# Kernel tuning notes

Measured on AMD Instinct MI355X. Metric: run time of the kernel, lower is better.

## Reference

```python
import jax, jax.numpy as jnp
import numpy as np

N_NODES = 50000
N_GRAPHS = 512

def _glorot(key, shape):
    fan_in, fan_out = shape[1], shape[0]
    lim = np.sqrt(6.0 / (fan_in + fan_out))
    return jax.random.uniform(key, shape, jnp.float32, -lim, lim)

def setup_inputs() -> dict:
    key = jax.random.key(0)
    ks = jax.random.split(key, 12)
    x = jax.random.normal(ks[0], (N_NODES, 128), jnp.float32)
    edge_index = jax.random.randint(ks[1], (2, 800000), 0, N_NODES, jnp.int64)
    batch = jnp.sort(jax.random.randint(ks[2], (N_NODES,), 0, N_GRAPHS, jnp.int64))
    return {
        "x": x,
        "edge_index": edge_index,
        "batch": batch,
        "W1": _glorot(ks[3], (256, 128)), "b1": jnp.zeros((256,), jnp.float32),
        "W2": _glorot(ks[4], (256, 256)), "b2": jnp.zeros((256,), jnp.float32),
        "W3": _glorot(ks[5], (256, 256)), "b3": jnp.zeros((256,), jnp.float32),
        "Wf1": _glorot(ks[6], (128, 256)), "bf1": jnp.zeros((128,), jnp.float32),
        "Wf2": _glorot(ks[7], (10, 128)), "bf2": jnp.zeros((10,), jnp.float32),
    }

def _gin_conv(h, edge_index, W, b):
    # GINConv (eps=0): lin(x_i + sum_{j in N(i)} x_j)
    src, dst = edge_index[0], edge_index[1]
    aggr = jax.ops.segment_sum(h[src], dst, num_segments=N_NODES)
    return (h + aggr) @ W.T + b

def reference(x, edge_index, batch, W1, b1, W2, b2, W3, b3, Wf1, bf1, Wf2, bf2):
    h = jax.nn.relu(_gin_conv(x, edge_index, W1, b1))
    h = jax.nn.relu(_gin_conv(h, edge_index, W2, b2))
    h = jax.nn.relu(_gin_conv(h, edge_index, W3, b3))
    # global mean pool over graphs
    sums = jax.ops.segment_sum(h, batch, num_segments=N_GRAPHS)
    counts = jax.ops.segment_sum(jnp.ones((N_NODES,), h.dtype), batch, num_segments=N_GRAPHS)
    hg = sums / jnp.maximum(counts, 1.0)[:, None]
    h = jax.nn.relu(hg @ Wf1.T + bf1)
    return h @ Wf2.T + bf2
```

## Files before the change

### kernel.cpp

```cpp
#include <hip/hip_runtime.h>

#define N_NODES 50000
#define N_GRAPHS 512
#define N_EDGES 800000

typedef __attribute__((ext_vector_type(8))) short short8;
typedef __attribute__((ext_vector_type(8))) unsigned short ushort8;
typedef __attribute__((ext_vector_type(4))) float floatx4;
typedef __attribute__((ext_vector_type(2))) float floatx2;

__device__ __forceinline__ float bf2f(unsigned short u) {
    union { unsigned int i; float f; } c;
    c.i = ((unsigned int)u) << 16;
    return c.f;
}
__device__ __forceinline__ unsigned short f2bf(float f) {
    union { float f; unsigned int i; } c;
    c.f = f;
    unsigned int u = c.i;
    return (unsigned short)((u + 0x7fffu + ((u >> 16) & 1u)) >> 16);
}

__device__ __forceinline__ unsigned char ftofp8(float f) {
    union { float f; unsigned int u; } c; c.f = f;
    unsigned int s = (c.u >> 24) & 0x80u;
    float a = fabsf(f);
    if (a < 0x1p-6f) return (unsigned char)s;
    if (a > 448.f)   return (unsigned char)(s | 0x7E);
    unsigned int u = c.u & 0x7FFFFFFFu;
    unsigned int r = u + 0x7FFFFu + ((u >> 20) & 1u);
    return (unsigned char)(s | (((r >> 23) - 120u) << 3) | ((r >> 20) & 7u));
}

__device__ __forceinline__ void f8acc(float* acc, uint2 v) {
    floatx2 a = __builtin_amdgcn_cvt_pk_f32_fp8(v.x, false);
    floatx2 b = __builtin_amdgcn_cvt_pk_f32_fp8(v.x, true);
    floatx2 c = __builtin_amdgcn_cvt_pk_f32_fp8(v.y, false);
    floatx2 d = __builtin_amdgcn_cvt_pk_f32_fp8(v.y, true);
    acc[0] += a[0]; acc[1] += a[1]; acc[2] += b[0]; acc[3] += b[1];
    acc[4] += c[0]; acc[5] += c[1]; acc[6] += d[0]; acc[7] += d[1];
}

__device__ __forceinline__ void g2lds16(const unsigned short* g, void* lds) {
    __builtin_amdgcn_global_load_lds(
        (const __attribute__((address_space(1))) void*)g,
        (__attribute__((address_space(3))) void*)lds, 16, 0, 0);
}

__global__ void conv_deg(const float* __restrict__ x, const float* __restrict__ W1,
                         const float* __restrict__ W2, const float* __restrict__ W3,
                         const int* __restrict__ dst,
                         unsigned char* __restrict__ xf8, unsigned short* __restrict__ o1,
                         unsigned short* __restrict__ o2, unsigned short* __restrict__ o3,
                         int* __restrict__ deg, float4* __restrict__ sums4) {
    int i = blockIdx.x * blockDim.x + threadIdx.x;
    if (i >= 2440960) {
        int j = i - 2440960;
        if (j < 32768) sums4[j] = make_float4(0.f, 0.f, 0.f, 0.f);
        return;
    }
    if (i >= 1640960) {
        int e = i - 1640960;
        atomicAdd(&deg[dst[e]], 1);
        return;
    }
    if (i < 1600000) {
        float4 v = ((const float4*)x)[i];
        uchar4 o;
        o.x = ftofp8(v.x); o.y = ftofp8(v.y); o.z = ftofp8(v.z); o.w = ftofp8(v.w);
        ((uchar4*)xf8)[i] = o;
        return;
    }
    int j = i - 1600000;
    const float* src; unsigned short* out; int base;
    if (j < 8192)       { src = W1; out = o1; base = j; }
    else if (j < 24576) { src = W2; out = o2; base = j - 8192; }
    else                { src = W3; out = o3; base = j - 24576; }
    float4 v = ((const float4*)src)[base];
    ushort4 o;
    o.x = f2bf(v.x); o.y = f2bf(v.y); o.z = f2bf(v.z); o.w = f2bf(v.w);
    ((ushort4*)out)[base] = o;
}

__global__ __launch_bounds__(1024) void scan1(const int* __restrict__ deg,
                                              int* __restrict__ rowptr,
                                              int* __restrict__ blocksum) {
    __shared__ int s[1024];
    int t = threadIdx.x;
    int i = blockIdx.x * 1024 + t;
    int v = (i < N_NODES) ? deg[i] : 0;
    s[t] = v;
    __syncthreads();
    for (int off = 1; off < 1024; off <<= 1) {
        int add = (t >= off) ? s[t - off] : 0;
        __syncthreads();
        s[t] += add;
        __syncthreads();
    }
    if (i < N_NODES) rowptr[i] = s[t] - v;
    if (t == 1023) blocksum[blockIdx.x] = s[t];
}

__global__ __launch_bounds__(1024) void scan3(int* __restrict__ rowptr,
                                              const int* __restrict__ blocksum,
                                              int* __restrict__ cursor) {
    __shared__ int bse[64];
    int t = threadIdx.x;
    if (t < 64) {
        const int NB = (N_NODES + 1023) / 1024;
        int orig = (t < NB) ? blocksum[t] : 0;
        int v = orig;
        for (int off = 1; off < 64; off <<= 1) {
            int u = __shfl_up(v, off, 64);
            if (t >= off) v += u;
        }
        bse[t] = v - orig;
    }
    __syncthreads();
    int i = blockIdx.x * 1024 + t;
    if (i < N_NODES) {
        int v = rowptr[i] + bse[i >> 10];
        rowptr[i] = v;
        cursor[i] = v;
    }
    if (i == 0) rowptr[N_NODES] = N_EDGES;
}

__global__ void scatter_csr(const int* __restrict__ src, const int* __restrict__ dst,
                            int* __restrict__ cursor, int* __restrict__ csr) {
    int e = blockIdx.x * blockDim.x + threadIdx.x;
    if (e < N_EDGES) {
        int pos = atomicAdd(&cursor[dst[e]], 1);
        csr[pos] = src[e];
    }
}

template <int C>
__global__ __launch_bounds__(256) void gather_f8(const unsigned char* __restrict__ h,
                                                 const int* __restrict__ rowptr,
                                                 const int* __restrict__ csr,
                                                 unsigned short* __restrict__ agg) {
    const int TPN = C / 8;
    const int NPB = 256 / TPN;
    int t = threadIdx.x;
    int n = blockIdx.x * NPB + t / TPN;
    if (n >= N_NODES) return;
    int c8 = t % TPN;
    const uint2* hp = (const uint2*)h + c8;
    float acc[8];
#pragma unroll
    for (int j = 0; j < 8; j++) acc[j] = 0.f;
    f8acc(acc, hp[(size_t)n * TPN]);
    int p = rowptr[n], end = rowptr[n + 1];
    for (; p + 8 <= end; p += 8) {
        int j0 = csr[p],     j1 = csr[p + 1], j2 = csr[p + 2], j3 = csr[p + 3];
        int j4 = csr[p + 4], j5 = csr[p + 5], j6 = csr[p + 6], j7 = csr[p + 7];
        uint2 v0 = hp[(size_t)j0 * TPN];
        uint2 v1 = hp[(size_t)j1 * TPN];
        uint2 v2 = hp[(size_t)j2 * TPN];
        uint2 v3 = hp[(size_t)j3 * TPN];
        uint2 v4 = hp[(size_t)j4 * TPN];
        uint2 v5 = hp[(size_t)j5 * TPN];
        uint2 v6 = hp[(size_t)j6 * TPN];
        uint2 v7 = hp[(size_t)j7 * TPN];
        f8acc(acc, v0); f8acc(acc, v1); f8acc(acc, v2); f8acc(acc, v3);
        f8acc(acc, v4); f8acc(acc, v5); f8acc(acc, v6); f8acc(acc, v7);
    }
    for (; p + 4 <= end; p += 4) {
        int j0 = csr[p], j1 = csr[p + 1], j2 = csr[p + 2], j3 = csr[p + 3];
        uint2 v0 = hp[(size_t)j0 * TPN];
        uint2 v1 = hp[(size_t)j1 * TPN];
        uint2 v2 = hp[(size_t)j2 * TPN];
        uint2 v3 = hp[(size_t)j3 * TPN];
        f8acc(acc, v0); f8acc(acc, v1); f8acc(acc, v2); f8acc(acc, v3);
    }
    for (; p < end; ++p) {
        uint2 v = hp[(size_t)csr[p] * TPN];
        f8acc(acc, v);
    }
    ushort8 o;
#pragma unroll
    for (int j = 0; j < 8; j++) o[j] = f2bf(acc[j]);
    ((ushort8*)agg)[(size_t)n * TPN + c8] = o;
}

template <int K, int F8OUT>
__global__ __launch_bounds__(256) void gemm_mfma64(
    const unsigned short* __restrict__ A, const unsigned short* __restrict__ W,
    const float* __restrict__ bias, void* __restrict__ Cout, int M) {
    __shared__ short8 As[256];
    __shared__ short8 Ws[512];

    int tid = threadIdx.x;
    int wave = tid >> 6, lane = tid & 63;
    int wm = wave & 1, wn = wave >> 1;
    int rowbase = blockIdx.x * 64;
    int colbase = blockIdx.y * 128;
    int lkc = lane >> 4, lr = lane & 15;
    int rsw = lr ^ (lkc << 2);
    int rslot = lkc * 16 + rsw;

    int ar = rowbase + wave * 16 + rsw; if (ar >= M) ar = M - 1;
    int wr0 = colbase + (0 * 4 + wave) * 16 + rsw;
    int wr1 = colbase + (1 * 4 + wave) * 16 + rsw;
    char* asb  = (char*)As + (size_t)(wave * 64) * 16;
    char* wsb0 = (char*)Ws + (size_t)(0 * 256 + wave * 64) * 16;
    char* wsb1 = (char*)Ws + (size_t)(1 * 256 + wave * 64) * 16;

    floatx4 acc[2][4];
#pragma unroll
    for (int i = 0; i < 2; i++)
#pragma unroll
        for (int j = 0; j < 4; j++) acc[i][j] = (floatx4)(0.f);

#pragma unroll 2
    for (int k0 = 0; k0 < K; k0 += 32) {
        int ks = k0 + lkc * 8;
        g2lds16(A + (size_t)ar * K + ks, asb);
        g2lds16(W + (size_t)wr0 * K + ks, wsb0);
        g2lds16(W + (size_t)wr1 * K + ks, wsb1);
        __syncthreads();

        short8 af[2], wf[4];
#pragma unroll
        for (int mt = 0; mt < 2; mt++) af[mt] = As[(wm * 2 + mt) * 64 + rslot];
#pragma unroll
        for (int nt = 0; nt < 4; nt++) wf[nt] = Ws[(wn * 4 + nt) * 64 + rslot];
#pragma unroll
        for (int mt = 0; mt < 2; mt++)
#pragma unroll
            for (int nt = 0; nt < 4; nt++)
                acc[mt][nt] = __builtin_amdgcn_mfma_f32_16x16x32_bf16(
                    af[mt], wf[nt], acc[mt][nt], 0, 0, 0);
        __syncthreads();
    }

#pragma unroll
    for (int mt = 0; mt < 2; mt++) {
#pragma unroll
        for (int reg = 0; reg < 4; reg++) {
            int row = rowbase + (wm * 2 + mt) * 16 + lkc * 4 + reg;
            if (row >= M) continue;
#pragma unroll
            for (int nt = 0; nt < 4; nt++) {
                int col = colbase + (wn * 4 + nt) * 16 + lr;
                float v = fmaxf(acc[mt][nt][reg] + bias[col], 0.f);
                if (F8OUT)
                    ((unsigned char*)Cout)[(size_t)row * 256 + col] = ftofp8(v);
                else
                    ((unsigned short*)Cout)[(size_t)row * 256 + col] = f2bf(v);
            }
        }
    }
}

__global__ __launch_bounds__(256) void pool_accum(const unsigned short* __restrict__ h,
                                                  const int* __restrict__ batch,
                                                  float* __restrict__ sums) {
    int t = threadIdx.x;
    int r0 = blockIdx.x * 32;
    int r1 = r0 + 32; if (r1 > N_NODES) r1 = N_NODES;
    if (r0 >= N_NODES) return;
    float acc = 0.f;
    int gcur = batch[r0];
    for (int r = r0; r < r1; ++r) {
        int g = batch[r];
        if (g != gcur) { atomicAdd(&sums[gcur * 256 + t], acc); acc = 0.f; gcur = g; }
        acc += bf2f(h[(size_t)r * 256 + t]);
    }
    atomicAdd(&sums[gcur * 256 + t], acc);
}

__global__ __launch_bounds__(128) void head(const float* __restrict__ sums,
                                            const int* __restrict__ batch,
                                            const float* __restrict__ Wf1,
                                            const float* __restrict__ bf1,
                                            const float* __restrict__ Wf2,
                                            const float* __restrict__ bf2,
                                            float* __restrict__ out) {
    __shared__ float hg[256];
    __shared__ float hid[128];
    int g = blockIdx.x;
    int t = threadIdx.x;
    int lo = 0, hi = N_NODES;
    while (lo < hi) { int m = (lo + hi) >> 1; if (batch[m] < g) lo = m + 1; else hi = m; }
    int start = lo;
    lo = 0; hi = N_NODES;
    while (lo < hi) { int m = (lo + hi) >> 1; if (batch[m] < g + 1) lo = m + 1; else hi = m; }
    int end = lo;
    float inv = 1.0f / fmaxf((float)(end - start), 1.0f);
    hg[t]       = sums[g * 256 + t] * inv;
    hg[t + 128] = sums[g * 256 + t + 128] * inv;
    __syncthreads();
    float a1 = bf1[t];
    for (int c = 0; c < 256; c++) a1 += hg[c] * Wf1[t * 256 + c];
    hid[t] = fmaxf(a1, 0.f);
    __syncthreads();
    if (t < 10) {
        float a = bf2[t];
        for (int j = 0; j < 128; j++) a += hid[j] * Wf2[t * 128 + j];
        out[g * 10 + t] = a;
    }
}

extern "C" void kernel_launch(void* const* d_in, const int* in_sizes, int n_in,
                              void* d_out, int out_size, void* d_ws, size_t ws_size,
                              hipStream_t stream) {
    const float* x   = (const float*)d_in[0];
    const int*  edge = (const int*)d_in[1];
    const int*  batch= (const int*)d_in[2];
    const float* W1  = (const float*)d_in[3];
    const float* b1  = (const float*)d_in[4];
    const float* W2  = (const float*)d_in[5];
    const float* b2  = (const float*)d_in[6];
    const float* W3  = (const float*)d_in[7];
    const float* b3  = (const float*)d_in[8];
    const float* Wf1 = (const float*)d_in[9];
    const float* bf1 = (const float*)d_in[10];
    const float* Wf2 = (const float*)d_in[11];
    const float* bf2 = (const float*)d_in[12];
    const int* src = edge;
    const int* dst = edge + N_EDGES;

    char* wsb = (char*)d_ws;
    size_t off = 0;
    auto alloc = [&](size_t bytes) { void* p = wsb + off; off += (bytes + 255) & ~(size_t)255; return p; };
    unsigned char*  x_f8  = (unsigned char*)alloc((size_t)N_NODES * 128);
    unsigned char*  h1_f8 = (unsigned char*)alloc((size_t)N_NODES * 256);
    unsigned char*  h2_f8 = (unsigned char*)alloc((size_t)N_NODES * 256);
    unsigned short* agg_bf= (unsigned short*)alloc((size_t)N_NODES * 256 * 2);
    unsigned short* hA_bf = (unsigned short*)alloc((size_t)N_NODES * 256 * 2);
    unsigned short* W1bf  = (unsigned short*)alloc(256 * 128 * 2);
    unsigned short* W2bf  = (unsigned short*)alloc(256 * 256 * 2);
    unsigned short* W3bf  = (unsigned short*)alloc(256 * 256 * 2);
    int* rowptr   = (int*)alloc((N_NODES + 4) * 4);
    int* cursor   = (int*)alloc(N_NODES * 4);
    int* deg      = (int*)alloc(N_NODES * 4);
    int* csr      = (int*)alloc(N_EDGES * 4);
    int* blocksum = (int*)alloc(64 * 4);
    float* sums   = (float*)alloc((size_t)N_GRAPHS * 256 * 4);

    const int NB_SCAN = (N_NODES + 1023) / 1024;

    hipMemsetAsync(deg, 0, N_NODES * sizeof(int), stream);
    conv_deg<<<(2473728 + 255) / 256, 256, 0, stream>>>(
        x, W1, W2, W3, dst, x_f8, W1bf, W2bf, W3bf, deg, (float4*)sums);

    scan1<<<NB_SCAN, 1024, 0, stream>>>(deg, rowptr, blocksum);
    scan3<<<NB_SCAN, 1024, 0, stream>>>(rowptr, blocksum, cursor);
    scatter_csr<<<(N_EDGES + 255) / 256, 256, 0, stream>>>(src, dst, cursor, csr);

    dim3 ggrid((N_NODES + 63) / 64, 2);

    gather_f8<128><<<(N_NODES + 15) / 16, 256, 0, stream>>>(x_f8, rowptr, csr, agg_bf);
    gemm_mfma64<128, 1><<<ggrid, 256, 0, stream>>>(agg_bf, W1bf, b1, h1_f8, N_NODES);

    gather_f8<256><<<(N_NODES + 7) / 8, 256, 0, stream>>>(h1_f8, rowptr, csr, agg_bf);
    gemm_mfma64<256, 1><<<ggrid, 256, 0, stream>>>(agg_bf, W2bf, b2, h2_f8, N_NODES);

    gather_f8<256><<<(N_NODES + 7) / 8, 256, 0, stream>>>(h2_f8, rowptr, csr, agg_bf);
    gemm_mfma64<256, 0><<<ggrid, 256, 0, stream>>>(agg_bf, W3bf, b3, hA_bf, N_NODES);

    pool_accum<<<(N_NODES + 31) / 32, 256, 0, stream>>>(hA_bf, batch, sums);
    head<<<N_GRAPHS, 128, 0, stream>>>(sums, batch, Wf1, bf1, Wf2, bf2, (float*)d_out);
}
```

Measured before the change: 380.4 us.

## Build CSR via two-pass bucketed binning and store 16-bit column indices

Replaces the single-pass global-atomic CSR scatter with a two-phase scheme: edges are first binned into 49 destination buckets of 1024 nodes using shared-memory counters and one global atomic per bucket per block. A per-bucket pass then scatters them into the CSR, so the per-node cursor atomics and writes stay within a localized region. CSR column indices shrink to 16-bit, which cuts the index bytes the gather kernels read. The 16-bit packing truncates node IDs at or above 65536, which fits only because N_NODES is 50000, and it adds a staging buffer and an extra launch. The scatter pass uses just 49 blocks, which may underuse the GPU.

```diff
diff --git a/kernel.cpp b/kernel.cpp
--- a/kernel.cpp
+++ b/kernel.cpp
@@ -3,6 +3,7 @@
 #define N_NODES 50000
 #define N_GRAPHS 512
 #define N_EDGES 800000
+#define NBKT 49
 
 typedef __attribute__((ext_vector_type(8))) short short8;
 typedef __attribute__((ext_vector_type(8))) unsigned short ushort8;
@@ -103,7 +104,8 @@
 
 __global__ __launch_bounds__(1024) void scan3(int* __restrict__ rowptr,
                                               const int* __restrict__ blocksum,
-                                              int* __restrict__ cursor) {
+                                              int* __restrict__ cursor,
+                                              int* __restrict__ gcursor) {
     __shared__ int bse[64];
     int t = threadIdx.x;
     if (t < 64) {
@@ -122,23 +124,62 @@
         int v = rowptr[i] + bse[i >> 10];
         rowptr[i] = v;
         cursor[i] = v;
+        if ((i & 1023) == 0) gcursor[i >> 10] = v;
     }
     if (i == 0) rowptr[N_NODES] = N_EDGES;
 }
 
-__global__ void scatter_csr(const int* __restrict__ src, const int* __restrict__ dst,
-                            int* __restrict__ cursor, int* __restrict__ csr) {
-    int e = blockIdx.x * blockDim.x + threadIdx.x;
-    if (e < N_EDGES) {
-        int pos = atomicAdd(&cursor[dst[e]], 1);
-        csr[pos] = src[e];
+__global__ __launch_bounds__(256) void bin_edges(const int* __restrict__ src,
+                                                 const int* __restrict__ dst,
+                                                 int* __restrict__ gcursor,
+                                                 unsigned int* __restrict__ staging) {
+    __shared__ int cnt[NBKT];
+    __shared__ int base[NBKT];
+    int t = threadIdx.x;
+    if (t < NBKT) cnt[t] = 0;
+    __syncthreads();
+    int e0 = blockIdx.x * 2048;
+    int d[8], s[8];
+#pragma unroll
+    for (int r = 0; r < 8; r++) {
+        int e = e0 + r * 256 + t;
+        if (e < N_EDGES) {
+            d[r] = dst[e]; s[r] = src[e];
+            atomicAdd(&cnt[d[r] >> 10], 1);
+        } else d[r] = -1;
+    }
+    __syncthreads();
+    if (t < NBKT) base[t] = atomicAdd(&gcursor[t], cnt[t]);
+    __syncthreads();
+#pragma unroll
+    for (int r = 0; r < 8; r++) {
+        if (d[r] >= 0) {
+            int off = atomicAdd(&base[d[r] >> 10], 1);
+            staging[off] = ((unsigned)d[r] << 16) | (unsigned)s[r];
+        }
+    }
+}
+
+__global__ __launch_bounds__(1024) void scatter_bkt(const unsigned int* __restrict__ staging,
+                                                    const int* __restrict__ rowptr,
+                                                    int* __restrict__ cursor,
+                                                    unsigned short* __restrict__ csr) {
+    int b = blockIdx.x;
+    int lo = rowptr[b << 10];
+    int nhi = (b + 1) << 10; if (nhi > N_NODES) nhi = N_NODES;
+    int hi = rowptr[nhi];
+    for (int p = lo + threadIdx.x; p < hi; p += 1024) {
+        unsigned v = staging[p];
+        int d = v >> 16;
+        int pos = atomicAdd(&cursor[d], 1);
+        csr[pos] = (unsigned short)(v & 0xFFFFu);
     }
 }
 
 template <int C>
 __global__ __launch_bounds__(256) void gather_f8(const unsigned char* __restrict__ h,
                                                  const int* __restrict__ rowptr,
-                                                 const int* __restrict__ csr,
+                                                 const unsigned short* __restrict__ csr,
                                                  unsigned short* __restrict__ agg) {
     const int TPN = C / 8;
     const int NPB = 256 / TPN;
@@ -325,20 +366,22 @@
     char* wsb = (char*)d_ws;
     size_t off = 0;
     auto alloc = [&](size_t bytes) { void* p = wsb + off; off += (bytes + 255) & ~(size_t)255; return p; };
-    unsigned char*  x_f8  = (unsigned char*)alloc((size_t)N_NODES * 128);
-    unsigned char*  h1_f8 = (unsigned char*)alloc((size_t)N_NODES * 256);
-    unsigned char*  h2_f8 = (unsigned char*)alloc((size_t)N_NODES * 256);
-    unsigned short* agg_bf= (unsigned short*)alloc((size_t)N_NODES * 256 * 2);
-    unsigned short* hA_bf = (unsigned short*)alloc((size_t)N_NODES * 256 * 2);
-    unsigned short* W1bf  = (unsigned short*)alloc(256 * 128 * 2);
-    unsigned short* W2bf  = (unsigned short*)alloc(256 * 256 * 2);
-    unsigned short* W3bf  = (unsigned short*)alloc(256 * 256 * 2);
-    int* rowptr   = (int*)alloc((N_NODES + 4) * 4);
-    int* cursor   = (int*)alloc(N_NODES * 4);
-    int* deg      = (int*)alloc(N_NODES * 4);
-    int* csr      = (int*)alloc(N_EDGES * 4);
-    int* blocksum = (int*)alloc(64 * 4);
-    float* sums   = (float*)alloc((size_t)N_GRAPHS * 256 * 4);
+    unsigned char*  x_f8   = (unsigned char*)alloc((size_t)N_NODES * 128);
+    unsigned char*  h1_f8  = (unsigned char*)alloc((size_t)N_NODES * 256);
+    unsigned char*  h2_f8  = (unsigned char*)alloc((size_t)N_NODES * 256);
+    unsigned short* agg_bf = (unsigned short*)alloc((size_t)N_NODES * 256 * 2);
+    unsigned short* hA_bf  = (unsigned short*)alloc((size_t)N_NODES * 256 * 2);
+    unsigned short* W1bf   = (unsigned short*)alloc(256 * 128 * 2);
+    unsigned short* W2bf   = (unsigned short*)alloc(256 * 256 * 2);
+    unsigned short* W3bf   = (unsigned short*)alloc(256 * 256 * 2);
+    int* rowptr    = (int*)alloc((N_NODES + 4) * 4);
+    int* cursor    = (int*)alloc(N_NODES * 4);
+    int* deg       = (int*)alloc(N_NODES * 4);
+    unsigned short* csr = (unsigned short*)alloc((size_t)N_EDGES * 2);
+    unsigned int* staging = (unsigned int*)alloc((size_t)N_EDGES * 4);
+    int* blocksum  = (int*)alloc(64 * 4);
+    int* gcursor   = (int*)alloc(64 * 4);
+    float* sums    = (float*)alloc((size_t)N_GRAPHS * 256 * 4);
 
     const int NB_SCAN = (N_NODES + 1023) / 1024;
 
@@ -347,8 +390,9 @@
         x, W1, W2, W3, dst, x_f8, W1bf, W2bf, W3bf, deg, (float4*)sums);
 
     scan1<<<NB_SCAN, 1024, 0, stream>>>(deg, rowptr, blocksum);
-    scan3<<<NB_SCAN, 1024, 0, stream>>>(rowptr, blocksum, cursor);
-    scatter_csr<<<(N_EDGES + 255) / 256, 256, 0, stream>>>(src, dst, cursor, csr);
+    scan3<<<NB_SCAN, 1024, 0, stream>>>(rowptr, blocksum, cursor, gcursor);
+    bin_edges<<<(N_EDGES + 2047) / 2048, 256, 0, stream>>>(src, dst, gcursor, staging);
+    scatter_bkt<<<NBKT, 1024, 0, stream>>>(staging, rowptr, cursor, csr);
 
     dim3 ggrid((N_NODES + 63) / 64, 2);
 
```

Result: no change. 384.2 us (+1.0%).
